# Kernel optimization log

Measured on AMD Instinct MI355X. Metric: run time of the kernel, lower is better.

The kernel has to match this reference:

```python
import jax, jax.numpy as jnp
import numpy as np

DEPTH = 4
SCALE = 1.0


def _exp_levels(v, depth):
    # Tensor-algebra exponential of a linear segment with increment v: level k = v^{(x)k} / k!
    # v: (B, C); returns tuple of (B, C^k) for k=1..depth
    B = v.shape[0]
    levels = [v]
    for k in range(2, depth + 1):
        levels.append((levels[-1][:, :, None] * v[:, None, :]).reshape(B, -1) / k)
    return tuple(levels)


def _chen_step(levels, v, depth):
    # Chen's identity: S_new = S (x) exp(v), flattened per level.
    e = _exp_levels(v, depth)
    B = v.shape[0]
    new = []
    for k in range(1, depth + 1):
        acc = levels[k - 1] + e[k - 1]
        for i in range(1, k):
            acc = acc + (levels[i - 1][:, :, None] * e[k - i - 1][:, None, :]).reshape(B, -1)
        new.append(acc)
    return tuple(new)


def signature(path, depth):
    # path: (B, T, C) -> concatenated signature levels (B, C + C^2 + ... + C^depth)
    dx = path[:, 1:] - path[:, :-1]          # (B, T-1, C)
    init = _exp_levels(dx[:, 0], depth)      # signature of first segment
    rest = jnp.moveaxis(dx[:, 1:], 0, 1)     # (T-2, B, C)

    def step(lv, v):
        return _chen_step(lv, v, depth), None

    final, _ = jax.lax.scan(step, init, rest)
    return jnp.concatenate(final, axis=-1)


def setup_inputs() -> dict:
    key = jax.random.key(0)
    k1, k2, k3 = jax.random.split(key, 3)
    N, B, T, C = 4096, 1024, 256, 10
    original = jax.random.normal(k1, (N, T, C), dtype=jnp.float32) * 0.1
    generated = jax.random.normal(k2, (B, T, C), dtype=jnp.float32) * 0.1
    sample_idx = jax.random.permutation(k3, N)[:B].astype(jnp.int64)  # sample without replacement
    return {"original": original, "generated": generated, "sample_idx": sample_idx}


def reference(original, generated, sample_idx):
    sig_orig = signature(original, DEPTH)                  # (N, D)
    selected = sig_orig[sample_idx]                        # (B, D)
    sig_gen = signature(generated, DEPTH)                  # (B, D)
    diff = jnp.mean(selected, axis=0) - jnp.mean(sig_gen, axis=0)
    return jnp.linalg.norm(diff) * SCALE
```

## Files before the change

kernel.cpp:

```cpp
#include <hip/hip_runtime.h>

#define T_LEN 256
#define C_DIM 10
#define NSTEP 255
#define BSZ   1024
#define NPAIR 1024
#define D1 10
#define D2 100
#define D3 1000
#define DTOT 11110
#define PATH_ELEMS (T_LEN * C_DIM)
#define DX_ELEMS (NSTEP * C_DIM)
#define DXROW 12

__global__ __launch_bounds__(512, 8) void sig_accum_kernel(
    const float* __restrict__ original,
    const float* __restrict__ generated,
    const int* __restrict__ sample_idx,
    float* __restrict__ ws, int nrep, int store_mode)
{
    const int tid = threadIdx.x;
    const int b   = blockIdx.x;

    __shared__ float s_dx[NSTEP * DXROW];

    const float* path_gen  = generated + (size_t)b * PATH_ELEMS;
    const float* path_orig = original + (size_t)sample_idx[b] * PATH_ELEMS;

    const int m0  = 2 * tid;
    const int k   = m0 / 100;
    const int ij0 = m0 - k * 100;
    const int ia  = ij0 / 10;
    const int j0  = ij0 - ia * 10;

    float s1a = 0.0f;
    float s2[2]  = {0.0f, 0.0f};
    float s3[2]  = {0.0f, 0.0f};
    float s2o[2] = {0.0f, 0.0f};
    float s3o[2] = {0.0f, 0.0f};
    float acc[2][10];
    #pragma unroll
    for (int q = 0; q < 2; ++q)
        #pragma unroll
        for (int l = 0; l < 10; ++l) acc[q][l] = 0.0f;

    #pragma unroll 1
    for (int pass = 0; pass < 2; ++pass) {
        const float* path = (pass == 0) ? path_gen : path_orig;

        for (int idx = tid; idx < DX_ELEMS; idx += 512) {
            int t = idx / C_DIM, c = idx - t * C_DIM;
            s_dx[t * DXROW + c] = path[idx + C_DIM] - path[idx];
        }
        __syncthreads();

        if (tid < 500) {
            const float* vrow = s_dx;
            #pragma unroll 1
            for (int t = 0; t < NSTEP; ++t, vrow += DXROW) {
                const float4 va = *(const float4*)(vrow);
                const float4 vb = *(const float4*)(vrow + 4);
                const float2 vc = *(const float2*)(vrow + 8);
                const float2 vjp = *(const float2*)(vrow + j0);
                const float via = vrow[ia];
                const float vk  = vrow[k];

                const float vv[10] = {va.x, va.y, va.z, va.w,
                                      vb.x, vb.y, vb.z, vb.w, vc.x, vc.y};
                const float vj[2] = {vjp.x, vjp.y};
                const float vkh = vk * 0.5f;
                const float t1 = s1a + via * 0.25f;
                const float t2 = s1a + via * (1.0f / 3.0f);
                const float t3 = s1a + via * 0.5f;

                #pragma unroll
                for (int q = 0; q < 2; ++q) {
                    const float a2 = s2[q] + t1 * (vj[q] * (1.0f / 3.0f));
                    const float b2 = s2[q] + t2 * (vj[q] * 0.5f);
                    s2[q]          = s2[q] + t3 * vj[q];
                    const float a3 = s3[q] + a2 * vkh;
                    s3[q] += b2 * vk;
                    #pragma unroll
                    for (int l = 0; l < 10; ++l) acc[q][l] += a3 * vv[l];
                }
                s1a += via;
            }
        }

        if (pass == 0) {
            #pragma unroll
            for (int q = 0; q < 2; ++q) {
                s2o[q] = -s2[q];  s2[q] = 0.0f;
                s3o[q] = -s3[q];  s3[q] = 0.0f;
                #pragma unroll
                for (int l = 0; l < 10; ++l) acc[q][l] = -acc[q][l];
            }
            s1a = 0.0f;
            __syncthreads();
        }
    }

    if (store_mode) {
        float* row = ws + (size_t)b * DTOT;
        if (tid < D1)
            row[tid] = (path_orig[(T_LEN - 1) * C_DIM + tid] - path_orig[tid])
                     - (path_gen[(T_LEN - 1) * C_DIM + tid] - path_gen[tid]);
        if (tid < 50) {
            row[D1 + ij0]     = s2o[0] + s2[0];
            row[D1 + ij0 + 1] = s2o[1] + s2[1];
        }
        if (tid < 500) {
            #pragma unroll
            for (int q = 0; q < 2; ++q) {
                const int idx3 = (ij0 + q) * 10 + k;
                row[D1 + D2 + idx3] = s3o[q] + s3[q];
                float* p4 = row + D1 + D2 + D3 + (size_t)idx3 * 10;
                #pragma unroll
                for (int l = 0; l < 10; l += 2)
                    *(float2*)&p4[l] = make_float2(acc[q][l], acc[q][l + 1]);
            }
        }
    } else {
        float* base = ws + (size_t)(b % nrep) * DTOT;
        if (tid < D1)
            atomicAdd(&base[tid],
                      (path_orig[(T_LEN - 1) * C_DIM + tid] - path_orig[tid])
                    - (path_gen[(T_LEN - 1) * C_DIM + tid] - path_gen[tid]));
        if (tid < 50) {
            atomicAdd(&base[D1 + ij0],     s2o[0] + s2[0]);
            atomicAdd(&base[D1 + ij0 + 1], s2o[1] + s2[1]);
        }
        if (tid < 500) {
            #pragma unroll
            for (int q = 0; q < 2; ++q) {
                const int idx3 = (ij0 + q) * 10 + k;
                atomicAdd(&base[D1 + D2 + idx3], s3o[q] + s3[q]);
                #pragma unroll
                for (int l = 0; l < 10; ++l)
                    atomicAdd(&base[D1 + D2 + D3 + idx3 * 10 + l], acc[q][l]);
            }
        }
    }
}

__global__ __launch_bounds__(256) void sig_sum_kernel(
    const float* __restrict__ ws, float* __restrict__ accvec)
{
    const int d2 = blockIdx.x * 256 + threadIdx.x;
    if (d2 >= DTOT / 2) return;
    const float* p = ws + (size_t)(blockIdx.y * 32) * DTOT + 2 * d2;
    float sx = 0.0f, sy = 0.0f;
    #pragma unroll
    for (int r = 0; r < 32; ++r) {
        const float2 v = *(const float2*)(p + (size_t)r * DTOT);
        sx += v.x; sy += v.y;
    }
    atomicAdd(&accvec[2 * d2], sx);
    atomicAdd(&accvec[2 * d2 + 1], sy);
}

__global__ __launch_bounds__(256) void sig_sumsq_kernel(
    const float* __restrict__ accvec, float* __restrict__ sumsq,
    unsigned int* __restrict__ counter, float* __restrict__ out, int nblocks)
{
    const int d = blockIdx.x * 256 + threadIdx.x;
    float s = 0.0f;
    if (d < DTOT) { float v = accvec[d]; s = v * v; }
    for (int off = 32; off > 0; off >>= 1) s += __shfl_down(s, off, 64);
    __shared__ float red[4];
    __shared__ unsigned int lastflag;
    if ((threadIdx.x & 63) == 0) red[threadIdx.x >> 6] = s;
    __syncthreads();
    if (threadIdx.x == 0) {
        atomicAdd(sumsq, red[0] + red[1] + red[2] + red[3]);
        __threadfence();
        lastflag = (atomicAdd(counter, 1u) == (unsigned int)(nblocks - 1));
    }
    __syncthreads();
    if (threadIdx.x == 0 && lastflag) {
        __threadfence();
        out[0] = sqrtf(*(volatile float*)sumsq) * (1.0f / (float)BSZ);
    }
}

__global__ __launch_bounds__(256) void sig_reduce_kernel(
    const float* __restrict__ ws, int nrows, float* __restrict__ sumsq,
    unsigned int* __restrict__ counter, float* __restrict__ out, int nblocks)
{
    const int d = blockIdx.x * 256 + threadIdx.x;
    float s = 0.0f;
    if (d < DTOT) {
        for (int r = 0; r < nrows; ++r) s += ws[(size_t)r * DTOT + d];
        s = s * s;
    }
    for (int off = 32; off > 0; off >>= 1) s += __shfl_down(s, off, 64);
    __shared__ float red[4];
    __shared__ unsigned int lastflag;
    if ((threadIdx.x & 63) == 0) red[threadIdx.x >> 6] = s;
    __syncthreads();
    if (threadIdx.x == 0) {
        atomicAdd(sumsq, red[0] + red[1] + red[2] + red[3]);
        __threadfence();
        lastflag = (atomicAdd(counter, 1u) == (unsigned int)(nblocks - 1));
    }
    __syncthreads();
    if (threadIdx.x == 0 && lastflag) {
        __threadfence();
        out[0] = sqrtf(*(volatile float*)sumsq) * (1.0f / (float)BSZ);
    }
}

extern "C" void kernel_launch(void* const* d_in, const int* in_sizes, int n_in,
                              void* d_out, int out_size, void* d_ws, size_t ws_size,
                              hipStream_t stream) {
    const float* original   = (const float*)d_in[0];
    const float* generated  = (const float*)d_in[1];
    const int*   sample_idx = (const int*)d_in[2];
    float* out = (float*)d_out;
    float* ws  = (float*)d_ws;

    const size_t need_store = ((size_t)(NPAIR + 1) * DTOT + 2) * sizeof(float);

    if (ws_size >= need_store) {
        float* accvec = ws + (size_t)NPAIR * DTOT;
        float* sumsq  = accvec + DTOT;
        unsigned int* counter = (unsigned int*)(sumsq + 1);
        hipMemsetAsync(accvec, 0, (DTOT + 2) * sizeof(float), stream);
        sig_accum_kernel<<<NPAIR, 512, 0, stream>>>(original, generated, sample_idx,
                                                    ws, 1, 1);
        dim3 g1((DTOT / 2 + 255) / 256, 32);
        sig_sum_kernel<<<g1, 256, 0, stream>>>(ws, accvec);
        const int nb2 = (DTOT + 255) / 256;
        sig_sumsq_kernel<<<nb2, 256, 0, stream>>>(accvec, sumsq, counter, out, nb2);
    } else {
        int nrep = 1;
        if (ws_size >= ((size_t)64 * DTOT + 2) * sizeof(float)) nrep = 64;
        else if (ws_size >= ((size_t)8 * DTOT + 2) * sizeof(float)) nrep = 8;
        float* sumsq = ws + (size_t)nrep * DTOT;
        unsigned int* counter = (unsigned int*)(sumsq + 1);
        hipMemsetAsync(ws, 0, ((size_t)nrep * DTOT + 2) * sizeof(float), stream);
        sig_accum_kernel<<<NPAIR, 512, 0, stream>>>(original, generated, sample_idx,
                                                    ws, nrep, 0);
        const int nb2 = (DTOT + 255) / 256;
        sig_reduce_kernel<<<nb2, 256, 0, stream>>>(ws, nrep, sumsq, counter, out, nb2);
    }
}
```

Baseline: 345.3 us.

## Coarsen signature threads to cover two level-3 indices each, using 256-thread blocks

Each thread now accumulates four level-3/level-4 entries, for k0 and k0+5, instead of two. The block shrinks to 256 threads and carries an amdgpu_waves_per_eu(4,4) hint. The per-step shared-memory loads of the increment row and the level-2 recurrences are now shared across twice as many outputs. This cuts LDS traffic and redundant scalar work per FMA. The cost is roughly double the accumulator registers per thread and half as many resident waves for hiding latency.

```diff
diff --git a/kernel.cpp b/kernel.cpp
--- a/kernel.cpp
+++ b/kernel.cpp
@@ -13,7 +13,9 @@
 #define DX_ELEMS (NSTEP * C_DIM)
 #define DXROW 12
 
-__global__ __launch_bounds__(512, 8) void sig_accum_kernel(
+__global__ __launch_bounds__(256)
+__attribute__((amdgpu_waves_per_eu(4, 4)))
+void sig_accum_kernel(
     const float* __restrict__ original,
     const float* __restrict__ generated,
     const int* __restrict__ sample_idx,
@@ -27,34 +29,34 @@
     const float* path_gen  = generated + (size_t)b * PATH_ELEMS;
     const float* path_orig = original + (size_t)sample_idx[b] * PATH_ELEMS;
 
-    const int m0  = 2 * tid;
-    const int k   = m0 / 100;
-    const int ij0 = m0 - k * 100;
+    const int mbase = 2 * tid;
+    const int k0  = mbase / 100;
+    const int ij0 = mbase - k0 * 100;
     const int ia  = ij0 / 10;
     const int j0  = ij0 - ia * 10;
 
     float s1a = 0.0f;
     float s2[2]  = {0.0f, 0.0f};
-    float s3[2]  = {0.0f, 0.0f};
     float s2o[2] = {0.0f, 0.0f};
-    float s3o[2] = {0.0f, 0.0f};
-    float acc[2][10];
+    float s3[4]  = {0.0f, 0.0f, 0.0f, 0.0f};
+    float s3o[4] = {0.0f, 0.0f, 0.0f, 0.0f};
+    float acc[4][10];
     #pragma unroll
-    for (int q = 0; q < 2; ++q)
+    for (int r = 0; r < 4; ++r)
         #pragma unroll
-        for (int l = 0; l < 10; ++l) acc[q][l] = 0.0f;
+        for (int l = 0; l < 10; ++l) acc[r][l] = 0.0f;
 
     #pragma unroll 1
     for (int pass = 0; pass < 2; ++pass) {
         const float* path = (pass == 0) ? path_gen : path_orig;
 
-        for (int idx = tid; idx < DX_ELEMS; idx += 512) {
+        for (int idx = tid; idx < DX_ELEMS; idx += 256) {
             int t = idx / C_DIM, c = idx - t * C_DIM;
             s_dx[t * DXROW + c] = path[idx + C_DIM] - path[idx];
         }
         __syncthreads();
 
-        if (tid < 500) {
+        if (tid < 250) {
             const float* vrow = s_dx;
             #pragma unroll 1
             for (int t = 0; t < NSTEP; ++t, vrow += DXROW) {
@@ -63,12 +65,14 @@
                 const float2 vc = *(const float2*)(vrow + 8);
                 const float2 vjp = *(const float2*)(vrow + j0);
                 const float via = vrow[ia];
-                const float vk  = vrow[k];
+                const float vk0 = vrow[k0];
+                const float vk1 = vrow[k0 + 5];
 
                 const float vv[10] = {va.x, va.y, va.z, va.w,
                                       vb.x, vb.y, vb.z, vb.w, vc.x, vc.y};
                 const float vj[2] = {vjp.x, vjp.y};
-                const float vkh = vk * 0.5f;
+                const float vk0h = vk0 * 0.5f;
+                const float vk1h = vk1 * 0.5f;
                 const float t1 = s1a + via * 0.25f;
                 const float t2 = s1a + via * (1.0f / 3.0f);
                 const float t3 = s1a + via * 0.5f;
@@ -78,10 +82,16 @@
                     const float a2 = s2[q] + t1 * (vj[q] * (1.0f / 3.0f));
                     const float b2 = s2[q] + t2 * (vj[q] * 0.5f);
                     s2[q]          = s2[q] + t3 * vj[q];
-                    const float a3 = s3[q] + a2 * vkh;
-                    s3[q] += b2 * vk;
-                    #pragma unroll
-                    for (int l = 0; l < 10; ++l) acc[q][l] += a3 * vv[l];
+
+                    const float a3x = s3[q] + a2 * vk0h;
+                    s3[q] += b2 * vk0;
+                    #pragma unroll
+                    for (int l = 0; l < 10; ++l) acc[q][l] += a3x * vv[l];
+
+                    const float a3y = s3[2 + q] + a2 * vk1h;
+                    s3[2 + q] += b2 * vk1;
+                    #pragma unroll
+                    for (int l = 0; l < 10; ++l) acc[2 + q][l] += a3y * vv[l];
                 }
                 s1a += via;
             }
@@ -89,11 +99,12 @@
 
         if (pass == 0) {
             #pragma unroll
-            for (int q = 0; q < 2; ++q) {
-                s2o[q] = -s2[q];  s2[q] = 0.0f;
-                s3o[q] = -s3[q];  s3[q] = 0.0f;
-                #pragma unroll
-                for (int l = 0; l < 10; ++l) acc[q][l] = -acc[q][l];
+            for (int q = 0; q < 2; ++q) { s2o[q] = -s2[q]; s2[q] = 0.0f; }
+            #pragma unroll
+            for (int r = 0; r < 4; ++r) {
+                s3o[r] = -s3[r];  s3[r] = 0.0f;
+                #pragma unroll
+                for (int l = 0; l < 10; ++l) acc[r][l] = -acc[r][l];
             }
             s1a = 0.0f;
             __syncthreads();
@@ -109,15 +120,20 @@
             row[D1 + ij0]     = s2o[0] + s2[0];
             row[D1 + ij0 + 1] = s2o[1] + s2[1];
         }
-        if (tid < 500) {
-            #pragma unroll
-            for (int q = 0; q < 2; ++q) {
-                const int idx3 = (ij0 + q) * 10 + k;
-                row[D1 + D2 + idx3] = s3o[q] + s3[q];
-                float* p4 = row + D1 + D2 + D3 + (size_t)idx3 * 10;
-                #pragma unroll
-                for (int l = 0; l < 10; l += 2)
-                    *(float2*)&p4[l] = make_float2(acc[q][l], acc[q][l + 1]);
+        if (tid < 250) {
+            #pragma unroll
+            for (int ch = 0; ch < 2; ++ch) {
+                const int kk = k0 + 5 * ch;
+                #pragma unroll
+                for (int q = 0; q < 2; ++q) {
+                    const int idx3 = (ij0 + q) * 10 + kk;
+                    row[D1 + D2 + idx3] = s3o[ch * 2 + q] + s3[ch * 2 + q];
+                    float* p4 = row + D1 + D2 + D3 + (size_t)idx3 * 10;
+                    #pragma unroll
+                    for (int l = 0; l < 10; l += 2)
+                        *(float2*)&p4[l] = make_float2(acc[ch * 2 + q][l],
+                                                       acc[ch * 2 + q][l + 1]);
+                }
             }
         }
     } else {
@@ -130,14 +146,19 @@
             atomicAdd(&base[D1 + ij0],     s2o[0] + s2[0]);
             atomicAdd(&base[D1 + ij0 + 1], s2o[1] + s2[1]);
         }
-        if (tid < 500) {
-            #pragma unroll
-            for (int q = 0; q < 2; ++q) {
-                const int idx3 = (ij0 + q) * 10 + k;
-                atomicAdd(&base[D1 + D2 + idx3], s3o[q] + s3[q]);
-                #pragma unroll
-                for (int l = 0; l < 10; ++l)
-                    atomicAdd(&base[D1 + D2 + D3 + idx3 * 10 + l], acc[q][l]);
+        if (tid < 250) {
+            #pragma unroll
+            for (int ch = 0; ch < 2; ++ch) {
+                const int kk = k0 + 5 * ch;
+                #pragma unroll
+                for (int q = 0; q < 2; ++q) {
+                    const int idx3 = (ij0 + q) * 10 + kk;
+                    atomicAdd(&base[D1 + D2 + idx3], s3o[ch * 2 + q] + s3[ch * 2 + q]);
+                    #pragma unroll
+                    for (int l = 0; l < 10; ++l)
+                        atomicAdd(&base[D1 + D2 + D3 + idx3 * 10 + l],
+                                  acc[ch * 2 + q][l]);
+                }
             }
         }
     }
@@ -226,7 +247,7 @@
         float* sumsq  = accvec + DTOT;
         unsigned int* counter = (unsigned int*)(sumsq + 1);
         hipMemsetAsync(accvec, 0, (DTOT + 2) * sizeof(float), stream);
-        sig_accum_kernel<<<NPAIR, 512, 0, stream>>>(original, generated, sample_idx,
+        sig_accum_kernel<<<NPAIR, 256, 0, stream>>>(original, generated, sample_idx,
                                                     ws, 1, 1);
         dim3 g1((DTOT / 2 + 255) / 256, 32);
         sig_sum_kernel<<<g1, 256, 0, stream>>>(ws, accvec);
@@ -239,7 +260,7 @@
         float* sumsq = ws + (size_t)nrep * DTOT;
         unsigned int* counter = (unsigned int*)(sumsq + 1);
         hipMemsetAsync(ws, 0, ((size_t)nrep * DTOT + 2) * sizeof(float), stream);
-        sig_accum_kernel<<<NPAIR, 512, 0, stream>>>(original, generated, sample_idx,
+        sig_accum_kernel<<<NPAIR, 256, 0, stream>>>(original, generated, sample_idx,
                                                     ws, nrep, 0);
         const int nb2 = (DTOT + 255) / 256;
         sig_reduce_kernel<<<nb2, 256, 0, stream>>>(ws, nrep, sumsq, counter, out, nb2);
```

After: 292.2 us. -15.4%, faster.
